# Kernel optimization log

Hardware: AMD Instinct MI355X
Metric: run time of the kernel (lower is better)

The kernel has to match this reference:

```python
import jax, jax.numpy as jnp
import numpy as np

B, J, D = 512, 22, 3
HIDDEN = 512
OUT = J * D          # 66, flattened frame size
NCLS = 12
LENGTH = 64


def setup_inputs() -> dict:
    key = jax.random.key(0)
    ks = jax.random.split(key, 12)
    s = 0.05
    return {
        "inputs": jax.random.normal(ks[0], (B, J, D), dtype=jnp.float32),
        "labels": jax.random.randint(ks[1], (B,), 0, NCLS),
        "length": LENGTH,
        # LSTMCell params (torch layout: W_ih [4H, in], W_hh [4H, H], gate order i,f,g,o)
        "W_ih": jax.random.normal(ks[2], (4 * HIDDEN, OUT + NCLS), dtype=jnp.float32) * s,
        "W_hh": jax.random.normal(ks[3], (4 * HIDDEN, HIDDEN), dtype=jnp.float32) * s,
        "b_ih": jax.random.normal(ks[4], (4 * HIDDEN,), dtype=jnp.float32) * s,
        "b_hh": jax.random.normal(ks[5], (4 * HIDDEN,), dtype=jnp.float32) * s,
        # fc: hidden -> output
        "W_fc": jax.random.normal(ks[6], (OUT, HIDDEN), dtype=jnp.float32) * s,
        "b_fc": jax.random.normal(ks[7], (OUT,), dtype=jnp.float32) * s,
        # fc_inh / fc_inc: output -> hidden (initial state projections)
        "W_inh": jax.random.normal(ks[8], (HIDDEN, OUT), dtype=jnp.float32) * s,
        "b_inh": jax.random.normal(ks[9], (HIDDEN,), dtype=jnp.float32) * s,
        "W_inc": jax.random.normal(ks[10], (HIDDEN, OUT), dtype=jnp.float32) * s,
        "b_inc": jax.random.normal(ks[11], (HIDDEN,), dtype=jnp.float32) * s,
    }


def reference(inputs, labels, length, W_ih, W_hh, b_ih, b_hh, W_fc, b_fc,
              W_inh, b_inh, W_inc, b_inc):
    b, j, d = inputs.shape
    enc = jax.nn.one_hot(labels, NCLS, dtype=inputs.dtype)      # [B, NCLS]
    frame0 = inputs.reshape(b, j * d)                            # [B, OUT]
    h0 = frame0 @ W_inh.T + b_inh                                # [B, H]
    c0 = frame0 @ W_inc.T + b_inc                                # [B, H]
    frame = jnp.concatenate([frame0, enc], axis=-1)              # [B, OUT+NCLS]

    def step(carry, _):
        h, c, fr = carry
        gates = fr @ W_ih.T + b_ih + h @ W_hh.T + b_hh           # [B, 4H]
        i, f, g, o = jnp.split(gates, 4, axis=-1)                # torch gate order
        c_new = jax.nn.sigmoid(f) * c + jax.nn.sigmoid(i) * jnp.tanh(g)
        h_new = jax.nn.sigmoid(o) * jnp.tanh(c_new)
        out = h_new @ W_fc.T + b_fc                              # [B, OUT]
        fr_new = jnp.concatenate([out, enc], axis=-1)
        return (h_new, c_new, fr_new), out

    _, outs = jax.lax.scan(step, (h0, c0, frame), None, length=length)  # [L, B, OUT]
    return jnp.transpose(outs, (1, 0, 2)).reshape(b, length, j, d)
```

## Files before the change

### kernel.cpp

```cpp
#include <hip/hip_runtime.h>

#define OUTD 66
#define INW  78
#define FH   2048
#define LEN  64

typedef short bf16x8 __attribute__((ext_vector_type(8)));
typedef float f32x4  __attribute__((ext_vector_type(4)));
typedef unsigned int u32x4 __attribute__((ext_vector_type(4)));

__device__ __forceinline__ float bf2f(unsigned short u) {
  union { unsigned int i; float f; } v; v.i = ((unsigned int)u) << 16; return v.f;
}
__device__ __forceinline__ unsigned short f2bf(float f) {
  union { float f; unsigned int i; } v; v.f = f;
  unsigned int u = v.i;
  return (unsigned short)((u + 0x7fffu + ((u >> 16) & 1u)) >> 16);
}
__device__ __forceinline__ float sigm(float x) { return 1.f / (1.f + __expf(-x)); }
__device__ __forceinline__ float tanh_f(float x) { return 2.f / (1.f + __expf(-2.f * x)) - 1.f; }

__device__ __forceinline__ unsigned int atom_or_ret(unsigned int* p, unsigned int d) {
  unsigned int r;
  asm volatile("global_atomic_or %0, %1, %2, off sc0\n\ts_waitcnt vmcnt(0)"
               : "=&v"(r) : "v"(p), "v"(d) : "memory");
  return r;
}
__device__ __forceinline__ void atom_or(unsigned int* p, unsigned int d) {
  asm volatile("global_atomic_or %0, %1, off" :: "v"(p), "v"(d) : "memory");
}

__global__ __launch_bounds__(256) void k_initA(
    const float* __restrict__ W_hh, const float* __restrict__ W_ih,
    const float* __restrict__ W_fc, const float* __restrict__ b_ih,
    const float* __restrict__ b_hh, const float* __restrict__ b_fc,
    const float* __restrict__ inp, const float* __restrict__ W_inh,
    const float* __restrict__ b_inh, const float* __restrict__ W_inc,
    const float* __restrict__ b_inc,
    unsigned short* __restrict__ Weff, float* __restrict__ bias_eff,
    unsigned short* __restrict__ hbuf, float* __restrict__ c0,
    unsigned short* __restrict__ Wfc16, unsigned int* __restrict__ flags,
    unsigned int* __restrict__ flagsL)
{
  int tid = threadIdx.x, bid = blockIdx.x;
  if (bid < 256) {
    int nb = bid;
    int k = tid * 2;
    float acc[8][2];
    #pragma unroll
    for (int r = 0; r < 8; ++r) {
      int n = nb * 8 + r;
      acc[r][0] = W_hh[n * 512 + k];
      acc[r][1] = W_hh[n * 512 + k + 1];
    }
    for (int m = 0; m < OUTD; ++m) {
      float w0 = W_fc[m * 512 + k];
      float w1 = W_fc[m * 512 + k + 1];
      #pragma unroll
      for (int r = 0; r < 8; ++r) {
        float wih = W_ih[(nb * 8 + r) * INW + m];
        acc[r][0] += wih * w0;
        acc[r][1] += wih * w1;
      }
    }
    #pragma unroll
    for (int r = 0; r < 8; ++r) {
      int n = nb * 8 + r;
      unsigned int pack = (unsigned int)f2bf(acc[r][0]) | ((unsigned int)f2bf(acc[r][1]) << 16);
      *(unsigned int*)(Weff + n * 512 + k) = pack;
    }
    if (tid < 8) {
      int n = nb * 8 + tid;
      float a = b_ih[n] + b_hh[n];
      for (int m = 0; m < OUTD; ++m) a += b_fc[m] * W_ih[n * INW + m];
      bias_eff[n] = a;
    }
    if (nb == 0) {
      for (int i = tid; i < 512 * 16; i += 256) flags[i] = 0;
      for (int i = tid; i < 256 * 16; i += 256) flagsL[i] = 0;
    }
  } else {
    int nb = bid - 256;
    for (int r = 0; r < 2; ++r) {
      int b = nb * 2 + r;
      for (int half = 0; half < 2; ++half) {
        int c = tid + half * 256;
        float ha = b_inh[c], ca = b_inc[c];
        for (int m = 0; m < OUTD; ++m) {
          float f = inp[b * OUTD + m];
          ha += f * W_inh[c * OUTD + m];
          ca += f * W_inc[c * OUTD + m];
        }
        hbuf[((b >> 5) * 32 + (c >> 4)) * 512 + (b & 31) * 16 + (c & 15)] = f2bf(ha);
        c0[b * 512 + c] = ca;
      }
    }
    if (nb == 0) {
      for (int i = tid; i < OUTD * 512; i += 256) Wfc16[i] = f2bf(W_fc[i]);
    }
  }
}

__global__ __launch_bounds__(128) void k_init2a(
    const float* __restrict__ inp, const unsigned short* __restrict__ hbuf,
    const float* __restrict__ W_fc, const float* __restrict__ b_fc,
    float* __restrict__ d0)
{
  int b = blockIdx.x, m = threadIdx.x;
  if (m >= OUTD) return;
  const unsigned short* hb = hbuf + (b >> 5) * 16384 + (b & 31) * 16;
  const float* wrow = W_fc + m * 512;
  float acc = 0.f;
  for (int k = 0; k < 512; ++k)
    acc += bf2f(hb[(k >> 4) * 512 + (k & 15)]) * wrow[k];
  d0[b * OUTD + m] = inp[b * OUTD + m] - (acc + b_fc[m]);
}

__global__ __launch_bounds__(256) void k_init2b(
    const float* __restrict__ d0, const float* __restrict__ W_ih,
    float* __restrict__ corr0)
{
  __shared__ float ds[4][OUTD];
  int tid = threadIdx.x, b0 = blockIdx.x * 4;
  for (int i = tid; i < 4 * OUTD; i += 256) ds[i / OUTD][i % OUTD] = d0[b0 * OUTD + i];
  __syncthreads();
  for (int n = tid; n < FH; n += 256) {
    float a0 = 0, a1 = 0, a2 = 0, a3 = 0;
    const float* wr = W_ih + n * INW;
    for (int m = 0; m < OUTD; ++m) {
      float w = wr[m];
      a0 += ds[0][m] * w; a1 += ds[1][m] * w; a2 += ds[2][m] * w; a3 += ds[3][m] * w;
    }
    corr0[(b0 + 0) * FH + n] = a0;
    corr0[(b0 + 1) * FH + n] = a1;
    corr0[(b0 + 2) * FH + n] = a2;
    corr0[(b0 + 3) * FH + n] = a3;
  }
}

__global__ __launch_bounds__(256, 2) void k_main(
    const unsigned short* __restrict__ Weff, const float* __restrict__ bias_eff,
    unsigned short* __restrict__ hbuf, const float* __restrict__ c0,
    const float* __restrict__ corr0, const float* __restrict__ W_ih,
    const int* __restrict__ labels, const unsigned short* __restrict__ Wfc16,
    const float* __restrict__ b_fc, float* __restrict__ out,
    unsigned int* __restrict__ flags, unsigned int* __restrict__ flagsL)
{
  __shared__ __align__(16) unsigned short h_lds[32 * 512];

  int tid = threadIdx.x, bid = blockIdx.x;
  int w = tid >> 6, lane = tid & 63;
  int lc = lane & 15, kg = lane >> 4;
  unsigned int* xmap = flags + 4608;
  unsigned int* decp = flags + 4100;
  unsigned int* maskW = flagsL;

  unsigned int xcd;
  asm volatile("s_getreg_b32 %0, hwreg(HW_REG_XCC_ID)" : "=s"(xcd));
  if (tid == 0)
    __hip_atomic_store(&xmap[bid * 4], xcd + 1u, __ATOMIC_RELAXED, __HIP_MEMORY_SCOPE_AGENT);

  if (bid == 0 && w == 0) {
    int okA = 1, okB = 1;
    #pragma unroll
    for (int i = 0; i < 8; ++i) {
      int b = lane + i * 64;
      unsigned int v, ra, rb;
      const unsigned int* xp = &xmap[b * 4];
      for (;;) { v = __hip_atomic_load(xp, __ATOMIC_RELAXED, __HIP_MEMORY_SCOPE_AGENT);
                 if (v) break; __builtin_amdgcn_s_sleep(1); }
      const unsigned int* pa = &xmap[(b & 15) * 4];
      for (;;) { ra = __hip_atomic_load(pa, __ATOMIC_RELAXED, __HIP_MEMORY_SCOPE_AGENT);
                 if (ra) break; __builtin_amdgcn_s_sleep(1); }
      const unsigned int* pb = &xmap[((b >> 5) << 5) * 4];
      for (;;) { rb = __hip_atomic_load(pb, __ATOMIC_RELAXED, __HIP_MEMORY_SCOPE_AGENT);
                 if (rb) break; __builtin_amdgcn_s_sleep(1); }
      okA &= (v == ra); okB &= (v == rb);
    }
    okA = __all(okA); okB = __all(okB);
    if (lane == 0) {
      unsigned int d = okA ? 1u : (okB ? 2u : 3u);
      __hip_atomic_store(decp, d, __ATOMIC_RELAXED, __HIP_MEMORY_SCOPE_AGENT);
    }
  }
  if (tid == 0) {
    unsigned int dd;
    for (;;) { dd = __hip_atomic_load(decp, __ATOMIC_RELAXED, __HIP_MEMORY_SCOPE_AGENT);
               if (dd) break; __builtin_amdgcn_s_sleep(1); }
    h_lds[0] = (unsigned short)dd;
  }
  __syncthreads();
  unsigned int dmode = h_lds[0];
  __syncthreads();

  int fast, mt, jt;
  if (dmode == 1u)      { fast = 1; mt = bid & 15;  jt = bid >> 4; }
  else if (dmode == 2u) { fast = 1; mt = bid >> 5;  jt = bid & 31; }
  else                  { fast = 0; mt = bid & 15;  jt = bid >> 4; }

  int row0 = mt * 32, j0 = jt * 16;
  int hx0 = (w >> 1) * 8;
  int xloc = lc & 7;
  int G = lc >> 3;
  int hcol = j0 + hx0 + xloc;
  int rw0 = (w & 1) * 16;

  int sA = xloc;
  int tA16 = ((kg ^ sA) & 3) << 4;
  int ue64 = ((sA >> 2) & 1) << 6;
  int PA0 = (rw0 + lc) * 1024 + tA16 + ue64;
  int PF  = ((w & 1) * 16 + lc) * 1024 + tA16 + ue64;

  bf16x8 Bfrag[16][2];
  #pragma unroll
  for (int cg = 0; cg < 2; ++cg) {
    int n = (cg * 2 + G) * 512 + hcol;
    const unsigned short* p = Weff + n * 512 + kg * 8;
    #pragma unroll
    for (int i = 0; i < 16; ++i) Bfrag[i][cg] = *(const bf16x8*)(p + i * 32);
  }

  bf16x8 Wf[16];
  float fcb = 0.f;
  {
    int n = j0 + lc;
    if (jt < 5 && w < 2 && n < OUTD) {
      const unsigned short* p = Wfc16 + n * 512 + kg * 8;
      #pragma unroll
      for (int i = 0; i < 16; ++i) Wf[i] = *(const bf16x8*)(p + i * 32);
      fcb = b_fc[n];
    } else {
      bf16x8 z8 = {0, 0, 0, 0, 0, 0, 0, 0};
      #pragma unroll
      for (int i = 0; i < 16; ++i) Wf[i] = z8;
    }
  }

  int qsel = G * 2;
  float lt[4][2], creg[2];
  #pragma unroll
  for (int idx = 0; idx < 2; ++idx) {
    int rloc = rw0 + kg * 4 + qsel + idx;
    int grow = row0 + rloc;
    int lab = labels[grow];
    #pragma unroll
    for (int gt = 0; gt < 4; ++gt) {
      int n = gt * 512 + hcol;
      lt[gt][idx] = bias_eff[n] + W_ih[n * INW + OUTD + lab];
    }
    creg[idx] = c0[grow * 512 + hcol];
  }

  const f32x4 z = {0.f, 0.f, 0.f, 0.f};
  unsigned int* myflag = &flags[(mt * 32 + jt) * 8];

  {
    const unsigned short* hsrc = hbuf + mt * 16384;
    #pragma unroll
    for (int i = 0; i < 8; ++i) {
      int n = tid + i * 256;
      int c = n >> 6, q = n & 63;
      int r = q >> 1, u = q & 1, g = c * 2 + u;
      *(u32x4*)(h_lds + r * 512 + ((g ^ (r & 7)) << 3)) =
          *(const u32x4*)(hsrc + n * 8);
    }
  }
  __syncthreads();

  f32x4 faP = z; int havP = 0, colP = 0;
  int dofcW = (jt < 5) & (w < 2);

  for (int s = 0; s < LEN; ++s) {
    if (havP) {
      int c = j0 + lc;
      if (c < OUTD) {
        #pragma unroll
        for (int q = 0; q < 4; ++q) {
          int b = row0 + (w & 1) * 16 + kg * 4 + q;
          out[((long)b * 64 + colP) * OUTD + c] = faP[q] + fcb;
        }
      }
      havP = 0;
    }

    f32x4 acc00 = z, acc01 = z;
    #pragma unroll
    for (int i = 0; i < 16; ++i) {
      bf16x8 a0 = *(const bf16x8*)((const char*)h_lds + (PA0 ^ (i << 6)));
      acc00 = __builtin_amdgcn_mfma_f32_16x16x32_bf16(a0, Bfrag[i][0], acc00, 0, 0, 0);
      acc01 = __builtin_amdgcn_mfma_f32_16x16x32_bf16(a0, Bfrag[i][1], acc01, 0, 0, 0);
    }

    f32x4 sh00, sh01;
    #pragma unroll
    for (int j = 0; j < 4; ++j) {
      sh00[j] = __shfl_xor(acc00[j], 8);
      sh01[j] = __shfl_xor(acc01[j], 8);
    }

    unsigned short hval[2];
    #pragma unroll
    for (int idx = 0; idx < 2; ++idx) {
      int qo = qsel + idx;
      float xi = (G ? sh00[qo] : acc00[qo]);
      float xf = (G ? acc00[qo] : sh00[qo]);
      float xg = (G ? sh01[qo] : acc01[qo]);
      float xo = (G ? acc01[qo] : sh01[qo]);
      xi += lt[0][idx]; xf += lt[1][idx]; xg += lt[2][idx]; xo += lt[3][idx];
      if (s == 0) {
        int rloc = rw0 + kg * 4 + qo;
        const float* cr = corr0 + (long)(row0 + rloc) * FH + hcol;
        xi += cr[0]; xf += cr[512]; xg += cr[1024]; xo += cr[1536];
      }
      float cn = sigm(xf) * creg[idx] + sigm(xi) * tanh_f(xg);
      creg[idx] = cn;
      hval[idx] = f2bf(sigm(xo) * tanh_f(cn));
    }

    unsigned int pkS = 0; int rlS = 0;
    {
      unsigned int* hdst32 = (unsigned int*)(hbuf + ((s + 1) & 1) * 262144);
      int base32 = (mt * 32 + jt) * 256;
      int ceL = (hx0 >> 1) + (xloc >> 1);
      int odd = xloc & 1;
      #pragma unroll
      for (int idx = 0; idx < 2; ++idx) {
        unsigned int mine = hval[idx];
        unsigned int part = (unsigned int)__shfl_xor((int)mine, 1);
        unsigned int p = odd ? (part | (mine << 16)) : (mine | (part << 16));
        if (idx == odd) { pkS = p; rlS = rw0 + kg * 4 + qsel + idx; }
      }
      if (fast) {
        hdst32[base32 + rlS * 8 + ceL] = pkS;
      } else {
        __hip_atomic_store(&hdst32[base32 + rlS * 8 + ceL], pkS,
                           __ATOMIC_RELAXED, __HIP_MEMORY_SCOPE_AGENT);
      }
    }

    __builtin_amdgcn_s_waitcnt(0);
    __syncthreads();
    if (tid == 0) {
      if (fast)
        atom_or(&maskW[(mt * 4 + (jt >> 3)) * 64 + s], 1u << (jt & 7));
      __hip_atomic_store(myflag, (unsigned int)(s + 1),
                         __ATOMIC_RELAXED, __HIP_MEMORY_SCOPE_AGENT);
    }

    int dofc = dofcW & (s >= 1);
    if (dofc) {
      f32x4 fa = z;
      #pragma unroll
      for (int i = 0; i < 16; ++i) {
        bf16x8 a = *(const bf16x8*)((const char*)h_lds + (PF ^ (i << 6)));
        fa = __builtin_amdgcn_mfma_f32_16x16x32_bf16(a, Wf[i], fa, 0, 0, 0);
      }
      faP = fa; havP = 1; colP = s - 1;
    }
    __syncthreads();

    {
      int gS = jt * 2 + (w >> 1);
      unsigned int* l32 = (unsigned int*)h_lds;
      l32[rlS * 256 + ((gS ^ (rlS & 7)) << 2) + (xloc >> 1)] = pkS;
    }

    if (s < LEN - 1 || jt < 5) {
      const unsigned short* hbC = hbuf + ((s + 1) & 1) * 262144 + mt * 16384;
      unsigned int mydone = (w == (jt >> 3)) ? (1u << (jt & 7)) : 0u;
      const unsigned int* fA = flags + (mt * 32 + w * 8 + (lane & 7)) * 8;
      unsigned int* mg = &maskW[(mt * 4 + w) * 64 + s];
      int agentMode = !fast;
      int spins = 0;
      while (mydone != 0xffu) {
        unsigned int avail;
        if (!agentMode) {
          unsigned int v = 0;
          if (lane == 0) v = atom_or_ret(mg, 0u);
          avail = (unsigned int)__shfl((int)v, 0);
          if (++spins > 1024) agentMode = 1;
        } else {
          unsigned int fv = __hip_atomic_load(fA, __ATOMIC_RELAXED, __HIP_MEMORY_SCOPE_AGENT);
          avail = (unsigned int)__ballot((int)(fv >= (unsigned int)(s + 1))) & 0xffu;
        }
        unsigned int todo = avail & ~mydone;
        if (!todo) { __builtin_amdgcn_s_sleep(1); continue; }

        if (agentMode)
          __builtin_amdgcn_fence(__ATOMIC_ACQUIRE, "agent");
        else
          asm volatile("buffer_inv\n\ts_waitcnt vmcnt(0)" ::: "memory");

        u32x4 ta[8];
        #pragma unroll
        for (int i = 0; i < 8; ++i) {
          if ((todo >> i) & 1u) {
            const unsigned short* cp = hbC + (w * 8 + i) * 512 + lane * 8;
            ta[i] = *(const u32x4*)cp;
          }
        }
        int r_ = lane >> 1, u = lane & 1;
        #pragma unroll
        for (int i = 0; i < 8; ++i) {
          if ((todo >> i) & 1u) {
            int c2 = (w * 8 + i) * 2 + u;
            *(u32x4*)(h_lds + r_ * 512 + ((c2 ^ (r_ & 7)) << 3)) = ta[i];
          }
        }
        mydone |= todo;
      }
    }
    __syncthreads();
  }

  if (dofcW) {
    int c = j0 + lc;
    if (havP && c < OUTD) {
      #pragma unroll
      for (int q = 0; q < 4; ++q) {
        int b = row0 + (w & 1) * 16 + kg * 4 + q;
        out[((long)b * 64 + colP) * OUTD + c] = faP[q] + fcb;
      }
    }
    f32x4 fa = z;
    #pragma unroll
    for (int i = 0; i < 16; ++i) {
      bf16x8 a = *(const bf16x8*)((const char*)h_lds + (PF ^ (i << 6)));
      fa = __builtin_amdgcn_mfma_f32_16x16x32_bf16(a, Wf[i], fa, 0, 0, 0);
    }
    if (c < OUTD) {
      #pragma unroll
      for (int q = 0; q < 4; ++q) {
        int b = row0 + (w & 1) * 16 + kg * 4 + q;
        out[((long)b * 64 + 63) * OUTD + c] = fa[q] + fcb;
      }
    }
  }
}

extern "C" void kernel_launch(void* const* d_in, const int* in_sizes, int n_in,
                              void* d_out, int out_size, void* d_ws, size_t ws_size,
                              hipStream_t stream) {
  (void)in_sizes; (void)n_in; (void)out_size; (void)ws_size;
  const float* inp   = (const float*)d_in[0];
  const int*   labels= (const int*)d_in[1];
  const float* W_ih  = (const float*)d_in[3];
  const float* W_hh  = (const float*)d_in[4];
  const float* b_ih  = (const float*)d_in[5];
  const float* b_hh  = (const float*)d_in[6];
  const float* W_fc  = (const float*)d_in[7];
  const float* b_fc  = (const float*)d_in[8];
  const float* W_inh = (const float*)d_in[9];
  const float* b_inh = (const float*)d_in[10];
  const float* W_inc = (const float*)d_in[11];
  const float* b_inc = (const float*)d_in[12];

  char* ws = (char*)d_ws;
  unsigned short* Weff = (unsigned short*)(ws + 0);
  float* bias_eff      = (float*)(ws + 2097152);
  unsigned short* hbuf = (unsigned short*)(ws + 2105344);
  float* c0            = (float*)(ws + 3153920);
  float* corr0         = (float*)(ws + 4202496);
  float* d0            = (float*)(ws + 8396800);
  unsigned int* flags  = (unsigned int*)(ws + 8531968);
  unsigned short* Wfc16= (unsigned short*)(ws + 8564736);
  unsigned int* flagsL = (unsigned int*)(ws + 8632320);

  k_initA<<<512, 256, 0, stream>>>(W_hh, W_ih, W_fc, b_ih, b_hh, b_fc,
                                   inp, W_inh, b_inh, W_inc, b_inc,
                                   Weff, bias_eff, hbuf, c0, Wfc16, flags, flagsL);
  k_init2a<<<512, 128, 0, stream>>>(inp, hbuf, W_fc, b_fc, d0);
  k_init2b<<<128, 256, 0, stream>>>(d0, W_ih, corr0);

  k_main<<<512, 256, 0, stream>>>(Weff, bias_eff, hbuf, c0, corr0, W_ih, labels,
                                  Wfc16, b_fc, (float*)d_out, flags, flagsL);
}
```

Baseline: 464.9 us.

## Replace per-wave bitmask polling with a per-group arrival counter barrier

Inter-block synchronization for the recurrent h exchange moves from per-wave atomic-OR bitmasks with incremental chunk gathering to a single atomic-add arrival counter per row group. The last arriver publishes a generation value. One wave polls it, then all waves load the full h tile at once. This removes the repeated per-wave atomic polling and the partial-copy loop, and drops the local write of the block's own h slice since it is reloaded from global. In exchange it gives up overlapping the gather with stragglers, and it relies on rotating counter resets across steps.

Result: faster. 427.3 us (-8.1%).

```diff
diff --git a/kernel.cpp b/kernel.cpp
--- a/kernel.cpp
+++ b/kernel.cpp
@@ -20,14 +20,11 @@
 __device__ __forceinline__ float sigm(float x) { return 1.f / (1.f + __expf(-x)); }
 __device__ __forceinline__ float tanh_f(float x) { return 2.f / (1.f + __expf(-2.f * x)) - 1.f; }
 
-__device__ __forceinline__ unsigned int atom_or_ret(unsigned int* p, unsigned int d) {
+__device__ __forceinline__ unsigned int atom_add_ret(unsigned int* p, unsigned int d) {
   unsigned int r;
-  asm volatile("global_atomic_or %0, %1, %2, off sc0\n\ts_waitcnt vmcnt(0)"
+  asm volatile("global_atomic_add %0, %1, %2, off sc0\n\ts_waitcnt vmcnt(0)"
                : "=&v"(r) : "v"(p), "v"(d) : "memory");
   return r;
-}
-__device__ __forceinline__ void atom_or(unsigned int* p, unsigned int d) {
-  asm volatile("global_atomic_or %0, %1, off" :: "v"(p), "v"(d) : "memory");
 }
 
 __global__ __launch_bounds__(256) void k_initA(
@@ -153,7 +150,6 @@
   int lc = lane & 15, kg = lane >> 4;
   unsigned int* xmap = flags + 4608;
   unsigned int* decp = flags + 4100;
-  unsigned int* maskW = flagsL;
 
   unsigned int xcd;
   asm volatile("s_getreg_b32 %0, hwreg(HW_REG_XCC_ID)" : "=s"(xcd));
@@ -253,6 +249,7 @@
 
   const f32x4 z = {0.f, 0.f, 0.f, 0.f};
   unsigned int* myflag = &flags[(mt * 32 + jt) * 8];
+  int agentMode = !fast;
 
   {
     const unsigned short* hsrc = hbuf + mt * 16384;
@@ -317,12 +314,12 @@
       hval[idx] = f2bf(sigm(xo) * tanh_f(cn));
     }
 
-    unsigned int pkS = 0; int rlS = 0;
     {
       unsigned int* hdst32 = (unsigned int*)(hbuf + ((s + 1) & 1) * 262144);
       int base32 = (mt * 32 + jt) * 256;
       int ceL = (hx0 >> 1) + (xloc >> 1);
       int odd = xloc & 1;
+      unsigned int pkS = 0; int rlS = 0;
       #pragma unroll
       for (int idx = 0; idx < 2; ++idx) {
         unsigned int mine = hval[idx];
@@ -340,9 +337,16 @@
 
     __builtin_amdgcn_s_waitcnt(0);
     __syncthreads();
-    if (tid == 0) {
-      if (fast)
-        atom_or(&maskW[(mt * 4 + (jt >> 3)) * 64 + s], 1u << (jt & 7));
+    if (tid == 128) {
+      if (fast) {
+        unsigned int* cntp = &flagsL[mt * 64 + ((s + 1) & 3)];
+        unsigned int old = atom_add_ret(cntp, 1u);
+        if (old == 31u) {
+          *(volatile unsigned int*)&flagsL[mt * 64 + 32 + ((s + 1) & 3)] =
+              (unsigned int)(s + 1);
+          *(volatile unsigned int*)&flagsL[mt * 64 + ((s + 3) & 3)] = 0u;
+        }
+      }
       __hip_atomic_store(myflag, (unsigned int)(s + 1),
                          __ATOMIC_RELAXED, __HIP_MEMORY_SCOPE_AGENT);
     }
@@ -357,57 +361,47 @@
       }
       faP = fa; havP = 1; colP = s - 1;
     }
+
+    int needE = (s < LEN - 1 || jt < 5);
+    if (w == 3 && needE) {
+      if (!agentMode) {
+        volatile const unsigned int* gop =
+            (volatile const unsigned int*)&flagsL[mt * 64 + 32 + ((s + 1) & 3)];
+        int spins = 0;
+        for (;;) {
+          asm volatile("buffer_inv\n\ts_waitcnt vmcnt(0)" ::: "memory");
+          if (*gop == (unsigned int)(s + 1)) break;
+          if (++spins > 1024) { agentMode = 1; break; }
+          __builtin_amdgcn_s_sleep(1);
+        }
+      }
+      if (agentMode) {
+        const unsigned int* fA = flags + (mt * 32 + (lane & 31)) * 8;
+        for (;;) {
+          unsigned int fv = __hip_atomic_load(fA, __ATOMIC_RELAXED, __HIP_MEMORY_SCOPE_AGENT);
+          if (__all((int)(fv >= (unsigned int)(s + 1)))) break;
+          __builtin_amdgcn_s_sleep(1);
+        }
+      }
+    }
     __syncthreads();
 
-    {
-      int gS = jt * 2 + (w >> 1);
-      unsigned int* l32 = (unsigned int*)h_lds;
-      l32[rlS * 256 + ((gS ^ (rlS & 7)) << 2) + (xloc >> 1)] = pkS;
-    }
-
-    if (s < LEN - 1 || jt < 5) {
+    if (needE) {
+      if (fast) {
+        asm volatile("buffer_inv\n\ts_waitcnt vmcnt(0)" ::: "memory");
+      } else {
+        __builtin_amdgcn_fence(__ATOMIC_ACQUIRE, "agent");
+      }
       const unsigned short* hbC = hbuf + ((s + 1) & 1) * 262144 + mt * 16384;
-      unsigned int mydone = (w == (jt >> 3)) ? (1u << (jt & 7)) : 0u;
-      const unsigned int* fA = flags + (mt * 32 + w * 8 + (lane & 7)) * 8;
-      unsigned int* mg = &maskW[(mt * 4 + w) * 64 + s];
-      int agentMode = !fast;
-      int spins = 0;
-      while (mydone != 0xffu) {
-        unsigned int avail;
-        if (!agentMode) {
-          unsigned int v = 0;
-          if (lane == 0) v = atom_or_ret(mg, 0u);
-          avail = (unsigned int)__shfl((int)v, 0);
-          if (++spins > 1024) agentMode = 1;
-        } else {
-          unsigned int fv = __hip_atomic_load(fA, __ATOMIC_RELAXED, __HIP_MEMORY_SCOPE_AGENT);
-          avail = (unsigned int)__ballot((int)(fv >= (unsigned int)(s + 1))) & 0xffu;
-        }
-        unsigned int todo = avail & ~mydone;
-        if (!todo) { __builtin_amdgcn_s_sleep(1); continue; }
-
-        if (agentMode)
-          __builtin_amdgcn_fence(__ATOMIC_ACQUIRE, "agent");
-        else
-          asm volatile("buffer_inv\n\ts_waitcnt vmcnt(0)" ::: "memory");
-
-        u32x4 ta[8];
-        #pragma unroll
-        for (int i = 0; i < 8; ++i) {
-          if ((todo >> i) & 1u) {
-            const unsigned short* cp = hbC + (w * 8 + i) * 512 + lane * 8;
-            ta[i] = *(const u32x4*)cp;
-          }
-        }
-        int r_ = lane >> 1, u = lane & 1;
-        #pragma unroll
-        for (int i = 0; i < 8; ++i) {
-          if ((todo >> i) & 1u) {
-            int c2 = (w * 8 + i) * 2 + u;
-            *(u32x4*)(h_lds + r_ * 512 + ((c2 ^ (r_ & 7)) << 3)) = ta[i];
-          }
-        }
-        mydone |= todo;
+      u32x4 ta[8];
+      #pragma unroll
+      for (int i = 0; i < 8; ++i)
+        ta[i] = *(const u32x4*)(hbC + (w * 8 + i) * 512 + lane * 8);
+      int r_ = lane >> 1, u = lane & 1;
+      #pragma unroll
+      for (int i = 0; i < 8; ++i) {
+        int c2 = (w * 8 + i) * 2 + u;
+        *(u32x4*)(h_lds + r_ * 512 + ((c2 ^ (r_ & 7)) << 3)) = ta[i];
       }
     }
     __syncthreads();
```
